# Kernel tuning notes

Measured on AMD Instinct MI355X. Metric: run time of the kernel, lower is better.

## Reference

```python
import jax, jax.numpy as jnp
import numpy as np

FEATURES = 1024
HEAD_DIM = 64
NUM_HEADS = 16
EPS = 1e-5


def setup_inputs() -> dict:
    key = jax.random.key(0)
    ks = jax.random.split(key, 6)
    x = jax.random.normal(ks[0], (2, 2048, FEATURES), dtype=jnp.float32)
    s_in = 1.0 / np.sqrt(FEATURES)
    s_hd = 1.0 / np.sqrt(NUM_HEADS * HEAD_DIM)
    return {
        "x": x,
        "gamma": jnp.ones((FEATURES,), jnp.float32),
        "beta": jnp.zeros((FEATURES,), jnp.float32),
        "Wq": jax.random.normal(ks[1], (FEATURES, NUM_HEADS * HEAD_DIM), jnp.float32) * s_in,
        "Wkv": jax.random.normal(ks[2], (FEATURES, 2 * HEAD_DIM), jnp.float32) * s_in,
        "Wo": jax.random.normal(ks[3], (NUM_HEADS * HEAD_DIM, FEATURES), jnp.float32) * s_hd,
        "bo": jax.random.normal(ks[4], (FEATURES,), jnp.float32) * s_hd,
    }


def reference(x, gamma, beta, Wq, Wkv, Wo, bo):
    # LayerNorm over last dim
    mu = jnp.mean(x, axis=-1, keepdims=True)
    var = jnp.mean(jnp.square(x - mu), axis=-1, keepdims=True)
    xn = (x - mu) * jax.lax.rsqrt(var + EPS) * gamma + beta

    b, t, _ = x.shape
    q = (xn @ Wq).reshape(b, t, NUM_HEADS, HEAD_DIM).transpose(0, 2, 1, 3)  # b h t d
    kv = xn @ Wkv  # b s 2d
    k, v = kv[..., :HEAD_DIM], kv[..., HEAD_DIM:]  # b s d (single shared head)

    scale = HEAD_DIM ** (-0.5)
    attn = jnp.einsum('bhtd,bsd->bhts', q, k) * scale
    attn = jax.nn.softmax(attn, axis=-1)
    out = jnp.einsum('bhts,bsd->bhtd', attn, v)
    out = out.transpose(0, 2, 1, 3).reshape(b, t, NUM_HEADS * HEAD_DIM)
    return out @ Wo + bo + x
```

## Files before the change

kernel.cpp:

```cpp
#include <hip/hip_runtime.h>

typedef __attribute__((ext_vector_type(8))) __bf16 bf16x8;
typedef __attribute__((ext_vector_type(4))) float floatx4;
typedef __attribute__((ext_vector_type(2))) unsigned int u32x2;
typedef unsigned short u16;
typedef unsigned int u32;

#define KSCALE 0.18033688011112042f

__device__ __forceinline__ u16 f2bf(float f) {
    union { float f; u32 u; } v; v.f = f;
    u32 r = v.u + 0x7fffu + ((v.u >> 16) & 1u);
    return (u16)(r >> 16);
}

__device__ __forceinline__ u32 pk2bf(float a, float b) {
    union { float f; u32 u; } x, y; x.f = a; y.f = b;
    return __builtin_amdgcn_perm(y.u + 0x8000u, x.u + 0x8000u, 0x07060302);
}

__device__ __forceinline__ void gl_lds16(const u16* g, u16* l) {
    __builtin_amdgcn_global_load_lds((const __attribute__((address_space(1))) void*)g,
                                     (__attribute__((address_space(3))) void*)l, 16, 0, 0);
}

__global__ __launch_bounds__(256) void transpose3(const float* __restrict__ Wq, const float* __restrict__ Wkv,
                                                  const float* __restrict__ Wo, u16* __restrict__ WqkvT,
                                                  u16* __restrict__ WoT) {
    const int z = blockIdx.z;
    const float* in = (z == 0) ? Wq : (z == 1 ? Wkv : Wo);
    u16* out = (z == 0) ? WqkvT : (z == 1 ? WqkvT + (size_t)1024 * 1024 : WoT);
    const int cols = (z == 1) ? 128 : 1024;
    const int tr = blockIdx.y * 64, tc = blockIdx.x * 64;
    if (tc >= cols) return;
    __shared__ float tile[64][68];
    const int t = threadIdx.x;
    for (int p = 0; p < 4; p++) {
        int ri = (t >> 4) + p * 16;
        int ci = (t & 15) * 4;
        float4 v = *(const float4*)&in[(size_t)(tr + ri) * cols + tc + ci];
        tile[ri][ci + 0] = v.x; tile[ri][ci + 1] = v.y;
        tile[ri][ci + 2] = v.z; tile[ri][ci + 3] = v.w;
    }
    __syncthreads();
    for (int p = 0; p < 4; p++) {
        int oc = (t >> 4) + p * 16;
        int ir = (t & 15) * 4;
        float s = (z == 1 && (tc + oc) < 64) ? KSCALE : 1.0f;
        ushort4 o;
        o.x = f2bf(tile[ir + 0][oc] * s);
        o.y = f2bf(tile[ir + 1][oc] * s);
        o.z = f2bf(tile[ir + 2][oc] * s);
        o.w = f2bf(tile[ir + 3][oc] * s);
        *(ushort4*)&out[(size_t)(tc + oc) * 1024 + tr + ir] = o;
    }
}

__global__ __launch_bounds__(256) void ln_kernel(const float* __restrict__ x, const float* __restrict__ gamma,
                                                 const float* __restrict__ beta, u16* __restrict__ xn) {
    const int row = blockIdx.x, t = threadIdx.x;
    const float* xr = x + (size_t)row * 1024;
    float4 v = *(const float4*)&xr[t * 4];
    float s = v.x + v.y + v.z + v.w;
    float s2 = v.x * v.x + v.y * v.y + v.z * v.z + v.w * v.w;
    for (int off = 1; off < 64; off <<= 1) {
        s += __shfl_xor(s, off, 64);
        s2 += __shfl_xor(s2, off, 64);
    }
    __shared__ float ps[4], ps2[4];
    int w = t >> 6, lane = t & 63;
    if (lane == 0) { ps[w] = s; ps2[w] = s2; }
    __syncthreads();
    float S = ps[0] + ps[1] + ps[2] + ps[3];
    float S2 = ps2[0] + ps2[1] + ps2[2] + ps2[3];
    float mu = S * (1.0f / 1024.0f);
    float var = S2 * (1.0f / 1024.0f) - mu * mu;
    float rstd = rsqrtf(var + 1e-5f);
    ushort4 o;
    o.x = f2bf((v.x - mu) * rstd * gamma[t * 4 + 0] + beta[t * 4 + 0]);
    o.y = f2bf((v.y - mu) * rstd * gamma[t * 4 + 1] + beta[t * 4 + 1]);
    o.z = f2bf((v.z - mu) * rstd * gamma[t * 4 + 2] + beta[t * 4 + 2]);
    o.w = f2bf((v.w - mu) * rstd * gamma[t * 4 + 3] + beta[t * 4 + 3]);
    *(ushort4*)&xn[(size_t)row * 1024 + t * 4] = o;
}

template <bool FINAL>
__global__ __launch_bounds__(256) void gemm_bt(const u16* __restrict__ A, const u16* __restrict__ BT,
                                               u16* __restrict__ Cb, float* __restrict__ Cf,
                                               const float* __restrict__ bias, const float* __restrict__ resid,
                                               int M, int N, int K) {
    __shared__ u16 as_[64 * 32];
    __shared__ u16 bs_[128 * 32];
    const int t = threadIdx.x;
    const int w = t >> 6, lane = t & 63, q = lane >> 4, c = lane & 15;
    const int tm = blockIdx.y * 64, tn = blockIdx.x * 128;
    const int wm = (w & 1) * 32, wn = (w >> 1) * 64;

    const int srow = lane >> 2, sch = lane & 3;
    const u16* ag = &A[(size_t)(tm + w * 16 + srow) * K + sch * 8];
    const u16* bg0 = &BT[(size_t)(tn + w * 32 + srow) * K + sch * 8];
    const u16* bg1 = &BT[(size_t)(tn + w * 32 + 16 + srow) * K + sch * 8];
    u16* al = &as_[(w * 16) * 32];
    u16* bl0 = &bs_[(w * 32) * 32];
    u16* bl1 = &bs_[(w * 32 + 16) * 32];

    floatx4 acc[2][4];
    for (int i = 0; i < 2; i++)
        for (int j = 0; j < 4; j++) acc[i][j] = (floatx4){0.f, 0.f, 0.f, 0.f};

    for (int k0 = 0; k0 < K; k0 += 32) {
        __syncthreads();
        gl_lds16(ag + k0, al);
        gl_lds16(bg0 + k0, bl0);
        gl_lds16(bg1 + k0, bl1);
        __syncthreads();
        bf16x8 af[2], bf[4];
#pragma unroll
        for (int i = 0; i < 2; i++) af[i] = *(const bf16x8*)&as_[(wm + i * 16 + c) * 32 + q * 8];
#pragma unroll
        for (int j = 0; j < 4; j++) bf[j] = *(const bf16x8*)&bs_[(wn + j * 16 + c) * 32 + q * 8];
#pragma unroll
        for (int i = 0; i < 2; i++)
#pragma unroll
            for (int j = 0; j < 4; j++)
                acc[i][j] = __builtin_amdgcn_mfma_f32_16x16x32_bf16(af[i], bf[j], acc[i][j], 0, 0, 0);
    }
#pragma unroll
    for (int i = 0; i < 2; i++)
#pragma unroll
        for (int j = 0; j < 4; j++)
#pragma unroll
            for (int r = 0; r < 4; r++) {
                int row = tm + wm + i * 16 + q * 4 + r;
                int col = tn + wn + j * 16 + c;
                if (FINAL)
                    Cf[(size_t)row * N + col] = acc[i][j][r] + bias[col] + resid[(size_t)row * N + col];
                else
                    Cb[(size_t)row * N + col] = f2bf(acc[i][j][r]);
            }
}

__global__ __launch_bounds__(256) void vt_prep(const u16* __restrict__ qkv, u16* __restrict__ vt) {
    __shared__ u16 tile[64][72];
    const int t = threadIdx.x;
    const int s0 = blockIdx.x * 64, b = blockIdx.y;
    for (int i = 0; i < 2; i++) {
        int ch = t + i * 256;
        int sl = ch >> 3, d0 = (ch & 7) * 8;
        *(uint4*)&tile[sl][d0] = *(const uint4*)&qkv[(size_t)(b * 2048 + s0 + sl) * 1152 + 1088 + d0];
    }
    __syncthreads();
    for (int i = 0; i < 2; i++) {
        int ch = t + i * 256;
        int d = ch >> 3, sl0 = (ch & 7) * 8;
        u16 tmp[8];
        for (int j = 0; j < 8; j++) tmp[j] = tile[sl0 + j][d];
        *(uint4*)&vt[((size_t)b * 64 + d) * 2048 + s0 + sl0] = *(uint4*)tmp;
    }
}

union Vf { bf16x8 v; u32 w[4]; };

__global__ __launch_bounds__(256, 2) void attn4(const u16* __restrict__ qkv, const u16* __restrict__ vt,
                                                u16* __restrict__ out) {
    __shared__ u16 ksm[2][64 * 64];
    __shared__ u16 vsm[2][64 * 64];
    const int t = threadIdx.x;
    const int w = t >> 6, lane = t & 63;
    const int q = lane >> 4, c = lane & 15;
    const int qt = blockIdx.x, hg = blockIdx.y, b = blockIdx.z;
    const int h = hg * 4 + w;
    const size_t qrow0 = (size_t)b * 2048 + qt * 32;
    const u16* kbase = qkv + (size_t)b * 2048 * 1152 + 1024;
    const u16* vbase = vt + (size_t)b * 64 * 2048;

    const int sr = w * 16 + (lane >> 3);
    const int sch = lane & 7;
    const int swz = (sch ^ (sr & 7)) * 8;
    const u16* kg0 = kbase + (size_t)sr * 1152 + swz;
    const u16* kg1 = kbase + (size_t)(sr + 8) * 1152 + swz;
    const u16* vg0 = vbase + (size_t)sr * 2048 + swz;
    const u16* vg1 = vbase + (size_t)(sr + 8) * 2048 + swz;
    u16* kl0[2] = {&ksm[0][(w * 16) * 64], &ksm[1][(w * 16) * 64]};
    u16* kl1[2] = {&ksm[0][(w * 16 + 8) * 64], &ksm[1][(w * 16 + 8) * 64]};
    u16* vl0[2] = {&vsm[0][(w * 16) * 64], &vsm[1][(w * 16) * 64]};
    u16* vl1[2] = {&vsm[0][(w * 16 + 8) * 64], &vsm[1][(w * 16 + 8) * 64]};

    bf16x8 qf[2][2];
#pragma unroll
    for (int mi = 0; mi < 2; mi++)
#pragma unroll
        for (int kk = 0; kk < 2; kk++)
            qf[mi][kk] = *(const bf16x8*)&qkv[(qrow0 + mi * 16 + c) * 1152 + h * 64 + kk * 32 + q * 8];

    floatx4 O[4][2], Lacc[2];
#pragma unroll
    for (int di = 0; di < 4; di++)
#pragma unroll
        for (int mi = 0; mi < 2; mi++) O[di][mi] = (floatx4){0.f, 0.f, 0.f, 0.f};
    Lacc[0] = (floatx4){0.f, 0.f, 0.f, 0.f};
    Lacc[1] = (floatx4){0.f, 0.f, 0.f, 0.f};
    Vf ones;
    ones.w[0] = ones.w[1] = ones.w[2] = ones.w[3] = 0x3F803F80u;

    gl_lds16(kg0, kl0[0]);
    gl_lds16(kg1, kl1[0]);
    gl_lds16(vg0, vl0[0]);
    gl_lds16(vg1, vl1[0]);
    __syncthreads();

    const int c7 = c & 7;
    for (int tt = 0; tt < 32; tt++) {
        const int cur = tt & 1, nxt = cur ^ 1;
        if (tt < 31) {
            const size_t ko = (size_t)(tt + 1) * 64 * 1152;
            const int vo = (tt + 1) * 64;
            gl_lds16(kg0 + ko, kl0[nxt]);
            gl_lds16(kg1 + ko, kl1[nxt]);
            gl_lds16(vg0 + vo, vl0[nxt]);
            gl_lds16(vg1 + vo, vl1[nxt]);
        }

        bf16x8 kf[4][2];
        Vf vf[4][2];
#pragma unroll
        for (int ni = 0; ni < 4; ni++)
#pragma unroll
            for (int kk = 0; kk < 2; kk++)
                kf[ni][kk] = *(const bf16x8*)&ksm[cur][(ni * 16 + c) * 64 + (((kk * 4 + q) ^ c7) * 8)];
#pragma unroll
        for (int di = 0; di < 4; di++)
#pragma unroll
            for (int kk = 0; kk < 2; kk++) {
                *(u32x2*)&vf[di][kk].w[0] =
                    *(const u32x2*)&vsm[cur][(di * 16 + c) * 64 + (((kk * 4 + (q >> 1)) ^ c7) * 8) + (q & 1) * 4];
                *(u32x2*)&vf[di][kk].w[2] =
                    *(const u32x2*)&vsm[cur][(di * 16 + c) * 64 + (((kk * 4 + 2 + (q >> 1)) ^ c7) * 8) + (q & 1) * 4];
            }

        floatx4 sacc[4][2];
#pragma unroll
        for (int ni = 0; ni < 4; ni++)
#pragma unroll
            for (int mi = 0; mi < 2; mi++) {
                floatx4 z = (floatx4){0.f, 0.f, 0.f, 0.f};
                z = __builtin_amdgcn_mfma_f32_16x16x32_bf16(kf[ni][0], qf[mi][0], z, 0, 0, 0);
                z = __builtin_amdgcn_mfma_f32_16x16x32_bf16(kf[ni][1], qf[mi][1], z, 0, 0, 0);
                sacc[ni][mi] = z;
            }

        u32 pk[4][2][2];
#pragma unroll
        for (int mi = 0; mi < 2; mi++)
#pragma unroll
            for (int ni = 0; ni < 4; ni++) {
                float p0 = exp2f(sacc[ni][mi][0]);
                float p1 = exp2f(sacc[ni][mi][1]);
                float p2 = exp2f(sacc[ni][mi][2]);
                float p3 = exp2f(sacc[ni][mi][3]);
                pk[ni][mi][0] = pk2bf(p0, p1);
                pk[ni][mi][1] = pk2bf(p2, p3);
            }

#pragma unroll
        for (int kk = 0; kk < 2; kk++) {
            Vf pf[2];
#pragma unroll
            for (int mi = 0; mi < 2; mi++) {
                pf[mi].w[0] = pk[2 * kk][mi][0];
                pf[mi].w[1] = pk[2 * kk][mi][1];
                pf[mi].w[2] = pk[2 * kk + 1][mi][0];
                pf[mi].w[3] = pk[2 * kk + 1][mi][1];
            }
#pragma unroll
            for (int di = 0; di < 4; di++)
#pragma unroll
                for (int mi = 0; mi < 2; mi++)
                    O[di][mi] = __builtin_amdgcn_mfma_f32_16x16x32_bf16(vf[di][kk].v, pf[mi].v, O[di][mi], 0, 0, 0);
#pragma unroll
            for (int mi = 0; mi < 2; mi++)
                Lacc[mi] = __builtin_amdgcn_mfma_f32_16x16x32_bf16(ones.v, pf[mi].v, Lacc[mi], 0, 0, 0);
        }

        __syncthreads();
    }

    float inv[2] = {1.0f / Lacc[0][0], 1.0f / Lacc[1][0]};
#pragma unroll
    for (int di = 0; di < 4; di++)
#pragma unroll
        for (int mi = 0; mi < 2; mi++) {
            ushort4 o;
            o.x = f2bf(O[di][mi][0] * inv[mi]);
            o.y = f2bf(O[di][mi][1] * inv[mi]);
            o.z = f2bf(O[di][mi][2] * inv[mi]);
            o.w = f2bf(O[di][mi][3] * inv[mi]);
            *(ushort4*)&out[(qrow0 + mi * 16 + c) * 1024 + h * 64 + di * 16 + q * 4] = o;
        }
}

extern "C" void kernel_launch(void* const* d_in, const int* in_sizes, int n_in,
                              void* d_out, int out_size, void* d_ws, size_t ws_size,
                              hipStream_t stream) {
    const float* x = (const float*)d_in[0];
    const float* gamma = (const float*)d_in[1];
    const float* beta = (const float*)d_in[2];
    const float* Wq = (const float*)d_in[3];
    const float* Wkv = (const float*)d_in[4];
    const float* Wo = (const float*)d_in[5];
    const float* bo = (const float*)d_in[6];
    float* out = (float*)d_out;

    u16* WqkvT = (u16*)d_ws;
    u16* WoT = WqkvT + (size_t)1152 * 1024;
    u16* xn = WoT + (size_t)1024 * 1024;
    u16* qkv = xn + (size_t)4096 * 1024;
    u16* attnO = xn;
    u16* Vt = WqkvT;

    transpose3<<<dim3(16, 16, 3), 256, 0, stream>>>(Wq, Wkv, Wo, WqkvT, WoT);
    ln_kernel<<<4096, 256, 0, stream>>>(x, gamma, beta, xn);
    gemm_bt<false><<<dim3(9, 64), 256, 0, stream>>>(xn, WqkvT, qkv, nullptr, nullptr, nullptr,
                                                    4096, 1152, 1024);
    vt_prep<<<dim3(32, 2), 256, 0, stream>>>(qkv, Vt);
    attn4<<<dim3(64, 4, 2), 256, 0, stream>>>(qkv, Vt, attnO);
    gemm_bt<true><<<dim3(8, 64), 256, 0, stream>>>(attnO, WoT, nullptr, out, bo, x,
                                                   4096, 1024, 1024);
}
```

Baseline: 199.2 us.

## Merge prep kernels, fuse V transpose into QKV GEMM, retile GEMM and attention

Combines the weight-transpose and LayerNorm kernels into one launch. The QKV GEMM epilogue now writes V directly into a permuted transposed layout, which removes the separate vt_prep kernel and its extra pass over V. The GEMM tile grows from 64x128 to 128x128 so each block does more MFMA work per B tile loaded. Attention moves to 512-thread blocks with 16 query rows per wave and a single 16-byte V fragment read, giving more waves per block and fewer LDS loads. The trade-offs are more accumulator registers in the GEMM and only half as many GEMM blocks.

```diff
diff --git a/kernel.cpp b/kernel.cpp
--- a/kernel.cpp
+++ b/kernel.cpp
@@ -2,7 +2,6 @@
 
 typedef __attribute__((ext_vector_type(8))) __bf16 bf16x8;
 typedef __attribute__((ext_vector_type(4))) float floatx4;
-typedef __attribute__((ext_vector_type(2))) unsigned int u32x2;
 typedef unsigned short u16;
 typedef unsigned int u32;
 
@@ -24,144 +23,138 @@
                                      (__attribute__((address_space(3))) void*)l, 16, 0, 0);
 }
 
-__global__ __launch_bounds__(256) void transpose3(const float* __restrict__ Wq, const float* __restrict__ Wkv,
-                                                  const float* __restrict__ Wo, u16* __restrict__ WqkvT,
-                                                  u16* __restrict__ WoT) {
-    const int z = blockIdx.z;
-    const float* in = (z == 0) ? Wq : (z == 1 ? Wkv : Wo);
-    u16* out = (z == 0) ? WqkvT : (z == 1 ? WqkvT + (size_t)1024 * 1024 : WoT);
-    const int cols = (z == 1) ? 128 : 1024;
-    const int tr = blockIdx.y * 64, tc = blockIdx.x * 64;
-    if (tc >= cols) return;
+__global__ __launch_bounds__(256) void prep(const float* __restrict__ Wq, const float* __restrict__ Wkv,
+                                            const float* __restrict__ Wo, const float* __restrict__ x,
+                                            const float* __restrict__ gamma, const float* __restrict__ beta,
+                                            u16* __restrict__ WqkvT, u16* __restrict__ WoT,
+                                            u16* __restrict__ xn) {
     __shared__ float tile[64][68];
+    __shared__ float ps[4], ps2[4];
+    const int bx = blockIdx.x;
     const int t = threadIdx.x;
-    for (int p = 0; p < 4; p++) {
-        int ri = (t >> 4) + p * 16;
-        int ci = (t & 15) * 4;
-        float4 v = *(const float4*)&in[(size_t)(tr + ri) * cols + tc + ci];
-        tile[ri][ci + 0] = v.x; tile[ri][ci + 1] = v.y;
-        tile[ri][ci + 2] = v.z; tile[ri][ci + 3] = v.w;
-    }
-    __syncthreads();
-    for (int p = 0; p < 4; p++) {
-        int oc = (t >> 4) + p * 16;
-        int ir = (t & 15) * 4;
-        float s = (z == 1 && (tc + oc) < 64) ? KSCALE : 1.0f;
+    if (bx < 768) {
+        const int z = bx >> 8, rem = bx & 255;
+        const int tr = (rem >> 4) * 64, tc = (rem & 15) * 64;
+        const float* in = (z == 0) ? Wq : (z == 1 ? Wkv : Wo);
+        u16* out = (z == 0) ? WqkvT : (z == 1 ? WqkvT + (size_t)1024 * 1024 : WoT);
+        const int cols = (z == 1) ? 128 : 1024;
+        if (tc >= cols) return;
+        for (int p = 0; p < 4; p++) {
+            int ri = (t >> 4) + p * 16;
+            int ci = (t & 15) * 4;
+            float4 v = *(const float4*)&in[(size_t)(tr + ri) * cols + tc + ci];
+            tile[ri][ci + 0] = v.x; tile[ri][ci + 1] = v.y;
+            tile[ri][ci + 2] = v.z; tile[ri][ci + 3] = v.w;
+        }
+        __syncthreads();
+        for (int p = 0; p < 4; p++) {
+            int oc = (t >> 4) + p * 16;
+            int ir = (t & 15) * 4;
+            float s = (z == 1 && (tc + oc) < 64) ? KSCALE : 1.0f;
+            ushort4 o;
+            o.x = f2bf(tile[ir + 0][oc] * s);
+            o.y = f2bf(tile[ir + 1][oc] * s);
+            o.z = f2bf(tile[ir + 2][oc] * s);
+            o.w = f2bf(tile[ir + 3][oc] * s);
+            *(ushort4*)&out[(size_t)(tc + oc) * 1024 + tr + ir] = o;
+        }
+    } else {
+        const int row = bx - 768;
+        const float* xr = x + (size_t)row * 1024;
+        float4 v = *(const float4*)&xr[t * 4];
+        float s = v.x + v.y + v.z + v.w;
+        float s2 = v.x * v.x + v.y * v.y + v.z * v.z + v.w * v.w;
+        for (int off = 1; off < 64; off <<= 1) {
+            s += __shfl_xor(s, off, 64);
+            s2 += __shfl_xor(s2, off, 64);
+        }
+        int w = t >> 6, lane = t & 63;
+        if (lane == 0) { ps[w] = s; ps2[w] = s2; }
+        __syncthreads();
+        float S = ps[0] + ps[1] + ps[2] + ps[3];
+        float S2 = ps2[0] + ps2[1] + ps2[2] + ps2[3];
+        float mu = S * (1.0f / 1024.0f);
+        float var = S2 * (1.0f / 1024.0f) - mu * mu;
+        float rstd = rsqrtf(var + 1e-5f);
         ushort4 o;
-        o.x = f2bf(tile[ir + 0][oc] * s);
-        o.y = f2bf(tile[ir + 1][oc] * s);
-        o.z = f2bf(tile[ir + 2][oc] * s);
-        o.w = f2bf(tile[ir + 3][oc] * s);
-        *(ushort4*)&out[(size_t)(tc + oc) * 1024 + tr + ir] = o;
-    }
-}
-
-__global__ __launch_bounds__(256) void ln_kernel(const float* __restrict__ x, const float* __restrict__ gamma,
-                                                 const float* __restrict__ beta, u16* __restrict__ xn) {
-    const int row = blockIdx.x, t = threadIdx.x;
-    const float* xr = x + (size_t)row * 1024;
-    float4 v = *(const float4*)&xr[t * 4];
-    float s = v.x + v.y + v.z + v.w;
-    float s2 = v.x * v.x + v.y * v.y + v.z * v.z + v.w * v.w;
-    for (int off = 1; off < 64; off <<= 1) {
-        s += __shfl_xor(s, off, 64);
-        s2 += __shfl_xor(s2, off, 64);
-    }
-    __shared__ float ps[4], ps2[4];
-    int w = t >> 6, lane = t & 63;
-    if (lane == 0) { ps[w] = s; ps2[w] = s2; }
-    __syncthreads();
-    float S = ps[0] + ps[1] + ps[2] + ps[3];
-    float S2 = ps2[0] + ps2[1] + ps2[2] + ps2[3];
-    float mu = S * (1.0f / 1024.0f);
-    float var = S2 * (1.0f / 1024.0f) - mu * mu;
-    float rstd = rsqrtf(var + 1e-5f);
-    ushort4 o;
-    o.x = f2bf((v.x - mu) * rstd * gamma[t * 4 + 0] + beta[t * 4 + 0]);
-    o.y = f2bf((v.y - mu) * rstd * gamma[t * 4 + 1] + beta[t * 4 + 1]);
-    o.z = f2bf((v.z - mu) * rstd * gamma[t * 4 + 2] + beta[t * 4 + 2]);
-    o.w = f2bf((v.w - mu) * rstd * gamma[t * 4 + 3] + beta[t * 4 + 3]);
-    *(ushort4*)&xn[(size_t)row * 1024 + t * 4] = o;
+        o.x = f2bf((v.x - mu) * rstd * gamma[t * 4 + 0] + beta[t * 4 + 0]);
+        o.y = f2bf((v.y - mu) * rstd * gamma[t * 4 + 1] + beta[t * 4 + 1]);
+        o.z = f2bf((v.z - mu) * rstd * gamma[t * 4 + 2] + beta[t * 4 + 2]);
+        o.w = f2bf((v.w - mu) * rstd * gamma[t * 4 + 3] + beta[t * 4 + 3]);
+        *(ushort4*)&xn[(size_t)row * 1024 + t * 4] = o;
+    }
 }
 
 template <bool FINAL>
 __global__ __launch_bounds__(256) void gemm_bt(const u16* __restrict__ A, const u16* __restrict__ BT,
                                                u16* __restrict__ Cb, float* __restrict__ Cf,
                                                const float* __restrict__ bias, const float* __restrict__ resid,
-                                               int M, int N, int K) {
-    __shared__ u16 as_[64 * 32];
+                                               u16* __restrict__ vt2, int M, int N, int K) {
+    __shared__ u16 as_[128 * 32];
     __shared__ u16 bs_[128 * 32];
     const int t = threadIdx.x;
     const int w = t >> 6, lane = t & 63, q = lane >> 4, c = lane & 15;
-    const int tm = blockIdx.y * 64, tn = blockIdx.x * 128;
-    const int wm = (w & 1) * 32, wn = (w >> 1) * 64;
-
-    const int srow = lane >> 2, sch = lane & 3;
-    const u16* ag = &A[(size_t)(tm + w * 16 + srow) * K + sch * 8];
-    const u16* bg0 = &BT[(size_t)(tn + w * 32 + srow) * K + sch * 8];
-    const u16* bg1 = &BT[(size_t)(tn + w * 32 + 16 + srow) * K + sch * 8];
-    u16* al = &as_[(w * 16) * 32];
-    u16* bl0 = &bs_[(w * 32) * 32];
-    u16* bl1 = &bs_[(w * 32 + 16) * 32];
-
-    floatx4 acc[2][4];
-    for (int i = 0; i < 2; i++)
+    const int tm = blockIdx.y * 128, tn = blockIdx.x * 128;
+    const int wm = (w & 1) * 64, wn = (w >> 1) * 64;
+
+    const int srow = lane >> 2, sch = (lane & 3) * 8;
+    const u16* ag0 = A + (size_t)(tm + w * 16 + srow) * K + sch;
+    const u16* ag1 = ag0 + (size_t)64 * K;
+    const u16* bg0 = BT + (size_t)(tn + w * 16 + srow) * K + sch;
+    const u16* bg1 = bg0 + (size_t)64 * K;
+    u16* al0 = as_ + (w * 16) * 32;
+    u16* al1 = as_ + (64 + w * 16) * 32;
+    u16* bl0 = bs_ + (w * 16) * 32;
+    u16* bl1 = bs_ + (64 + w * 16) * 32;
+
+    floatx4 acc[4][4];
+    for (int i = 0; i < 4; i++)
         for (int j = 0; j < 4; j++) acc[i][j] = (floatx4){0.f, 0.f, 0.f, 0.f};
 
     for (int k0 = 0; k0 < K; k0 += 32) {
         __syncthreads();
-        gl_lds16(ag + k0, al);
+        gl_lds16(ag0 + k0, al0);
+        gl_lds16(ag1 + k0, al1);
         gl_lds16(bg0 + k0, bl0);
         gl_lds16(bg1 + k0, bl1);
         __syncthreads();
-        bf16x8 af[2], bf[4];
-#pragma unroll
-        for (int i = 0; i < 2; i++) af[i] = *(const bf16x8*)&as_[(wm + i * 16 + c) * 32 + q * 8];
+        bf16x8 af[4], bf[4];
+#pragma unroll
+        for (int i = 0; i < 4; i++) af[i] = *(const bf16x8*)&as_[(wm + i * 16 + c) * 32 + q * 8];
 #pragma unroll
         for (int j = 0; j < 4; j++) bf[j] = *(const bf16x8*)&bs_[(wn + j * 16 + c) * 32 + q * 8];
 #pragma unroll
-        for (int i = 0; i < 2; i++)
+        for (int i = 0; i < 4; i++)
 #pragma unroll
             for (int j = 0; j < 4; j++)
                 acc[i][j] = __builtin_amdgcn_mfma_f32_16x16x32_bf16(af[i], bf[j], acc[i][j], 0, 0, 0);
     }
 #pragma unroll
-    for (int i = 0; i < 2; i++)
+    for (int i = 0; i < 4; i++)
 #pragma unroll
         for (int j = 0; j < 4; j++)
 #pragma unroll
             for (int r = 0; r < 4; r++) {
                 int row = tm + wm + i * 16 + q * 4 + r;
                 int col = tn + wn + j * 16 + c;
-                if (FINAL)
-                    Cf[(size_t)row * N + col] = acc[i][j][r] + bias[col] + resid[(size_t)row * N + col];
-                else
-                    Cb[(size_t)row * N + col] = f2bf(acc[i][j][r]);
+                float v = acc[i][j][r];
+                if (FINAL) {
+                    Cf[(size_t)row * N + col] = v + bias[col] + resid[(size_t)row * N + col];
+                } else if (col < 1088) {
+                    Cb[(size_t)row * N + col] = f2bf(v);
+                } else {
+                    int d = col - 1088;
+                    int bb = row >> 11, sl = row & 2047;
+                    int Bk = sl >> 5, u = sl & 31;
+                    int up = ((u >> 2) & 3) * 8 + ((u >> 4) << 2) + (u & 3);
+                    vt2[((size_t)(bb * 64 + d)) * 2048 + Bk * 32 + up] = f2bf(v);
+                }
             }
 }
 
-__global__ __launch_bounds__(256) void vt_prep(const u16* __restrict__ qkv, u16* __restrict__ vt) {
-    __shared__ u16 tile[64][72];
-    const int t = threadIdx.x;
-    const int s0 = blockIdx.x * 64, b = blockIdx.y;
-    for (int i = 0; i < 2; i++) {
-        int ch = t + i * 256;
-        int sl = ch >> 3, d0 = (ch & 7) * 8;
-        *(uint4*)&tile[sl][d0] = *(const uint4*)&qkv[(size_t)(b * 2048 + s0 + sl) * 1152 + 1088 + d0];
-    }
-    __syncthreads();
-    for (int i = 0; i < 2; i++) {
-        int ch = t + i * 256;
-        int d = ch >> 3, sl0 = (ch & 7) * 8;
-        u16 tmp[8];
-        for (int j = 0; j < 8; j++) tmp[j] = tile[sl0 + j][d];
-        *(uint4*)&vt[((size_t)b * 64 + d) * 2048 + s0 + sl0] = *(uint4*)tmp;
-    }
-}
-
 union Vf { bf16x8 v; u32 w[4]; };
 
-__global__ __launch_bounds__(256, 2) void attn4(const u16* __restrict__ qkv, const u16* __restrict__ vt,
+__global__ __launch_bounds__(512, 4) void attn5(const u16* __restrict__ qkv, const u16* __restrict__ vt2,
                                                 u16* __restrict__ out) {
     __shared__ u16 ksm[2][64 * 64];
     __shared__ u16 vsm[2][64 * 64];
@@ -169,56 +162,41 @@
     const int w = t >> 6, lane = t & 63;
     const int q = lane >> 4, c = lane & 15;
     const int qt = blockIdx.x, hg = blockIdx.y, b = blockIdx.z;
-    const int h = hg * 4 + w;
-    const size_t qrow0 = (size_t)b * 2048 + qt * 32;
+    const int h = hg * 8 + w;
+    const size_t qrow0 = (size_t)b * 2048 + qt * 16;
     const u16* kbase = qkv + (size_t)b * 2048 * 1152 + 1024;
-    const u16* vbase = vt + (size_t)b * 64 * 2048;
-
-    const int sr = w * 16 + (lane >> 3);
+    const u16* vbase = vt2 + (size_t)b * 64 * 2048;
+
+    const int srow = w * 8 + (lane >> 3);
     const int sch = lane & 7;
-    const int swz = (sch ^ (sr & 7)) * 8;
-    const u16* kg0 = kbase + (size_t)sr * 1152 + swz;
-    const u16* kg1 = kbase + (size_t)(sr + 8) * 1152 + swz;
-    const u16* vg0 = vbase + (size_t)sr * 2048 + swz;
-    const u16* vg1 = vbase + (size_t)(sr + 8) * 2048 + swz;
-    u16* kl0[2] = {&ksm[0][(w * 16) * 64], &ksm[1][(w * 16) * 64]};
-    u16* kl1[2] = {&ksm[0][(w * 16 + 8) * 64], &ksm[1][(w * 16 + 8) * 64]};
-    u16* vl0[2] = {&vsm[0][(w * 16) * 64], &vsm[1][(w * 16) * 64]};
-    u16* vl1[2] = {&vsm[0][(w * 16 + 8) * 64], &vsm[1][(w * 16 + 8) * 64]};
-
-    bf16x8 qf[2][2];
-#pragma unroll
-    for (int mi = 0; mi < 2; mi++)
-#pragma unroll
-        for (int kk = 0; kk < 2; kk++)
-            qf[mi][kk] = *(const bf16x8*)&qkv[(qrow0 + mi * 16 + c) * 1152 + h * 64 + kk * 32 + q * 8];
-
-    floatx4 O[4][2], Lacc[2];
-#pragma unroll
-    for (int di = 0; di < 4; di++)
-#pragma unroll
-        for (int mi = 0; mi < 2; mi++) O[di][mi] = (floatx4){0.f, 0.f, 0.f, 0.f};
-    Lacc[0] = (floatx4){0.f, 0.f, 0.f, 0.f};
-    Lacc[1] = (floatx4){0.f, 0.f, 0.f, 0.f};
+    const int swz = (sch ^ (srow & 7)) * 8;
+    const u16* kg = kbase + (size_t)srow * 1152 + swz;
+    const u16* vg = vbase + (size_t)srow * 2048 + swz;
+    u16* kl[2] = {&ksm[0][(w * 8) * 64], &ksm[1][(w * 8) * 64]};
+    u16* vl[2] = {&vsm[0][(w * 8) * 64], &vsm[1][(w * 8) * 64]};
+
+    bf16x8 qf[2];
+#pragma unroll
+    for (int kk = 0; kk < 2; kk++)
+        qf[kk] = *(const bf16x8*)&qkv[(qrow0 + c) * 1152 + h * 64 + kk * 32 + q * 8];
+
+    floatx4 O[4], Lacc;
+#pragma unroll
+    for (int di = 0; di < 4; di++) O[di] = (floatx4){0.f, 0.f, 0.f, 0.f};
+    Lacc = (floatx4){0.f, 0.f, 0.f, 0.f};
     Vf ones;
     ones.w[0] = ones.w[1] = ones.w[2] = ones.w[3] = 0x3F803F80u;
 
-    gl_lds16(kg0, kl0[0]);
-    gl_lds16(kg1, kl1[0]);
-    gl_lds16(vg0, vl0[0]);
-    gl_lds16(vg1, vl1[0]);
+    gl_lds16(kg, kl[0]);
+    gl_lds16(vg, vl[0]);
     __syncthreads();
 
     const int c7 = c & 7;
     for (int tt = 0; tt < 32; tt++) {
         const int cur = tt & 1, nxt = cur ^ 1;
         if (tt < 31) {
-            const size_t ko = (size_t)(tt + 1) * 64 * 1152;
-            const int vo = (tt + 1) * 64;
-            gl_lds16(kg0 + ko, kl0[nxt]);
-            gl_lds16(kg1 + ko, kl1[nxt]);
-            gl_lds16(vg0 + vo, vl0[nxt]);
-            gl_lds16(vg1 + vo, vl1[nxt]);
+            gl_lds16(kg + (size_t)(tt + 1) * 64 * 1152, kl[nxt]);
+            gl_lds16(vg + (tt + 1) * 64, vl[nxt]);
         }
 
         bf16x8 kf[4][2];
@@ -231,72 +209,55 @@
 #pragma unroll
         for (int di = 0; di < 4; di++)
 #pragma unroll
-            for (int kk = 0; kk < 2; kk++) {
-                *(u32x2*)&vf[di][kk].w[0] =
-                    *(const u32x2*)&vsm[cur][(di * 16 + c) * 64 + (((kk * 4 + (q >> 1)) ^ c7) * 8) + (q & 1) * 4];
-                *(u32x2*)&vf[di][kk].w[2] =
-                    *(const u32x2*)&vsm[cur][(di * 16 + c) * 64 + (((kk * 4 + 2 + (q >> 1)) ^ c7) * 8) + (q & 1) * 4];
-            }
-
-        floatx4 sacc[4][2];
-#pragma unroll
-        for (int ni = 0; ni < 4; ni++)
-#pragma unroll
-            for (int mi = 0; mi < 2; mi++) {
-                floatx4 z = (floatx4){0.f, 0.f, 0.f, 0.f};
-                z = __builtin_amdgcn_mfma_f32_16x16x32_bf16(kf[ni][0], qf[mi][0], z, 0, 0, 0);
-                z = __builtin_amdgcn_mfma_f32_16x16x32_bf16(kf[ni][1], qf[mi][1], z, 0, 0, 0);
-                sacc[ni][mi] = z;
-            }
-
-        u32 pk[4][2][2];
-#pragma unroll
-        for (int mi = 0; mi < 2; mi++)
-#pragma unroll
-            for (int ni = 0; ni < 4; ni++) {
-                float p0 = exp2f(sacc[ni][mi][0]);
-                float p1 = exp2f(sacc[ni][mi][1]);
-                float p2 = exp2f(sacc[ni][mi][2]);
-                float p3 = exp2f(sacc[ni][mi][3]);
-                pk[ni][mi][0] = pk2bf(p0, p1);
-                pk[ni][mi][1] = pk2bf(p2, p3);
-            }
+            for (int kk = 0; kk < 2; kk++)
+                vf[di][kk].v = *(const bf16x8*)&vsm[cur][(di * 16 + c) * 64 + (((kk * 4 + q) ^ c7) * 8)];
+
+        floatx4 sacc[4];
+#pragma unroll
+        for (int ni = 0; ni < 4; ni++) {
+            floatx4 z = (floatx4){0.f, 0.f, 0.f, 0.f};
+            z = __builtin_amdgcn_mfma_f32_16x16x32_bf16(kf[ni][0], qf[0], z, 0, 0, 0);
+            z = __builtin_amdgcn_mfma_f32_16x16x32_bf16(kf[ni][1], qf[1], z, 0, 0, 0);
+            sacc[ni] = z;
+        }
+
+        u32 pk[4][2];
+#pragma unroll
+        for (int ni = 0; ni < 4; ni++) {
+            float p0 = exp2f(sacc[ni][0]);
+            float p1 = exp2f(sacc[ni][1]);
+            float p2 = exp2f(sacc[ni][2]);
+            float p3 = exp2f(sacc[ni][3]);
+            pk[ni][0] = pk2bf(p0, p1);
+            pk[ni][1] = pk2bf(p2, p3);
+        }
 
 #pragma unroll
         for (int kk = 0; kk < 2; kk++) {
-            Vf pf[2];
-#pragma unroll
-            for (int mi = 0; mi < 2; mi++) {
-                pf[mi].w[0] = pk[2 * kk][mi][0];
-                pf[mi].w[1] = pk[2 * kk][mi][1];
-                pf[mi].w[2] = pk[2 * kk + 1][mi][0];
-                pf[mi].w[3] = pk[2 * kk + 1][mi][1];
-            }
+            Vf pf;
+            pf.w[0] = pk[2 * kk][0];
+            pf.w[1] = pk[2 * kk][1];
+            pf.w[2] = pk[2 * kk + 1][0];
+            pf.w[3] = pk[2 * kk + 1][1];
 #pragma unroll
             for (int di = 0; di < 4; di++)
-#pragma unroll
-                for (int mi = 0; mi < 2; mi++)
-                    O[di][mi] = __builtin_amdgcn_mfma_f32_16x16x32_bf16(vf[di][kk].v, pf[mi].v, O[di][mi], 0, 0, 0);
-#pragma unroll
-            for (int mi = 0; mi < 2; mi++)
-                Lacc[mi] = __builtin_amdgcn_mfma_f32_16x16x32_bf16(ones.v, pf[mi].v, Lacc[mi], 0, 0, 0);
-        }
-
-        __syncthreads();
-    }
-
-    float inv[2] = {1.0f / Lacc[0][0], 1.0f / Lacc[1][0]};
-#pragma unroll
-    for (int di = 0; di < 4; di++)
-#pragma unroll
-        for (int mi = 0; mi < 2; mi++) {
-            ushort4 o;
-            o.x = f2bf(O[di][mi][0] * inv[mi]);
-            o.y = f2bf(O[di][mi][1] * inv[mi]);
-            o.z = f2bf(O[di][mi][2] * inv[mi]);
-            o.w = f2bf(O[di][mi][3] * inv[mi]);
-            *(ushort4*)&out[(qrow0 + mi * 16 + c) * 1024 + h * 64 + di * 16 + q * 4] = o;
-        }
+                O[di] = __builtin_amdgcn_mfma_f32_16x16x32_bf16(vf[di][kk].v, pf.v, O[di], 0, 0, 0);
+            Lacc = __builtin_amdgcn_mfma_f32_16x16x32_bf16(ones.v, pf.v, Lacc, 0, 0, 0);
+        }
+
+        __syncthreads();
+    }
+
+    float inv = 1.0f / Lacc[0];
+#pragma unroll
+    for (int di = 0; di < 4; di++) {
+        ushort4 o;
+        o.x = f2bf(O[di][0] * inv);
+        o.y = f2bf(O[di][1] * inv);
+        o.z = f2bf(O[di][2] * inv);
+        o.w = f2bf(O[di][3] * inv);
+        *(ushort4*)&out[(qrow0 + c) * 1024 + h * 64 + di * 16 + q * 4] = o;
+    }
 }
 
 extern "C" void kernel_launch(void* const* d_in, const int* in_sizes, int n_in,
@@ -315,15 +276,13 @@
     u16* WoT = WqkvT + (size_t)1152 * 1024;
     u16* xn = WoT + (size_t)1024 * 1024;
     u16* qkv = xn + (size_t)4096 * 1024;
+    u16* vt2 = qkv + (size_t)4096 * 1152;
     u16* attnO = xn;
-    u16* Vt = WqkvT;
-
-    transpose3<<<dim3(16, 16, 3), 256, 0, stream>>>(Wq, Wkv, Wo, WqkvT, WoT);
-    ln_kernel<<<4096, 256, 0, stream>>>(x, gamma, beta, xn);
-    gemm_bt<false><<<dim3(9, 64), 256, 0, stream>>>(xn, WqkvT, qkv, nullptr, nullptr, nullptr,
+
+    prep<<<4864, 256, 0, stream>>>(Wq, Wkv, Wo, x, gamma, beta, WqkvT, WoT, xn);
+    gemm_bt<false><<<dim3(9, 32), 256, 0, stream>>>(xn, WqkvT, qkv, nullptr, nullptr, nullptr, vt2,
                                                     4096, 1152, 1024);
-    vt_prep<<<dim3(32, 2), 256, 0, stream>>>(qkv, Vt);
-    attn4<<<dim3(64, 4, 2), 256, 0, stream>>>(qkv, Vt, attnO);
-    gemm_bt<true><<<dim3(8, 64), 256, 0, stream>>>(attnO, WoT, nullptr, out, bo, x,
+    attn5<<<dim3(128, 2, 2), 512, 0, stream>>>(qkv, vt2, attnO);
+    gemm_bt<true><<<dim3(8, 32), 256, 0, stream>>>(attnO, WoT, nullptr, out, bo, x, nullptr,
                                                    4096, 1024, 1024);
 }
```

After: 199.9 us. No clear change (+0.4%).

## Fuse prep kernels, widen GEMM K-tile with swizzle, emit permuted V^T from QKV GEMM

Applied to the files above, without the earlier changes.

Merges the weight transpose and LayerNorm into one prep launch. The GEMM now loads 64-wide K tiles with an XOR-swizzled LDS layout, halving barrier count per K. The QKV GEMM epilogue writes V directly in a transposed, permuted layout, so the separate vt_prep kernel goes away and attention can read V fragments with single 16-byte LDS loads. This cuts launches and a pass over V. In exchange it adds scattered 2-byte stores in the V epilogue and doubles LDS per GEMM block, which may lower occupancy.

```diff
diff --git a/kernel.cpp b/kernel.cpp
--- a/kernel.cpp
+++ b/kernel.cpp
@@ -2,7 +2,6 @@
 
 typedef __attribute__((ext_vector_type(8))) __bf16 bf16x8;
 typedef __attribute__((ext_vector_type(4))) float floatx4;
-typedef __attribute__((ext_vector_type(2))) unsigned int u32x2;
 typedef unsigned short u16;
 typedef unsigned int u32;
 
@@ -24,106 +23,130 @@
                                      (__attribute__((address_space(3))) void*)l, 16, 0, 0);
 }
 
-__global__ __launch_bounds__(256) void transpose3(const float* __restrict__ Wq, const float* __restrict__ Wkv,
-                                                  const float* __restrict__ Wo, u16* __restrict__ WqkvT,
-                                                  u16* __restrict__ WoT) {
-    const int z = blockIdx.z;
-    const float* in = (z == 0) ? Wq : (z == 1 ? Wkv : Wo);
-    u16* out = (z == 0) ? WqkvT : (z == 1 ? WqkvT + (size_t)1024 * 1024 : WoT);
-    const int cols = (z == 1) ? 128 : 1024;
-    const int tr = blockIdx.y * 64, tc = blockIdx.x * 64;
-    if (tc >= cols) return;
+__global__ __launch_bounds__(256) void prep(const float* __restrict__ Wq, const float* __restrict__ Wkv,
+                                            const float* __restrict__ Wo, const float* __restrict__ x,
+                                            const float* __restrict__ gamma, const float* __restrict__ beta,
+                                            u16* __restrict__ WqkvT, u16* __restrict__ WoT,
+                                            u16* __restrict__ xn) {
     __shared__ float tile[64][68];
+    __shared__ float ps[4], ps2[4];
+    const int bx = blockIdx.x;
     const int t = threadIdx.x;
-    for (int p = 0; p < 4; p++) {
-        int ri = (t >> 4) + p * 16;
-        int ci = (t & 15) * 4;
-        float4 v = *(const float4*)&in[(size_t)(tr + ri) * cols + tc + ci];
-        tile[ri][ci + 0] = v.x; tile[ri][ci + 1] = v.y;
-        tile[ri][ci + 2] = v.z; tile[ri][ci + 3] = v.w;
+    if (bx < 768) {
+        const int z = bx >> 8, rem = bx & 255;
+        const int tr = (rem >> 4) * 64, tc = (rem & 15) * 64;
+        const float* in = (z == 0) ? Wq : (z == 1 ? Wkv : Wo);
+        u16* out = (z == 0) ? WqkvT : (z == 1 ? WqkvT + (size_t)1024 * 1024 : WoT);
+        const int cols = (z == 1) ? 128 : 1024;
+        if (tc >= cols) return;
+        for (int p = 0; p < 4; p++) {
+            int ri = (t >> 4) + p * 16;
+            int ci = (t & 15) * 4;
+            float4 v = *(const float4*)&in[(size_t)(tr + ri) * cols + tc + ci];
+            tile[ri][ci + 0] = v.x; tile[ri][ci + 1] = v.y;
+            tile[ri][ci + 2] = v.z; tile[ri][ci + 3] = v.w;
+        }
+        __syncthreads();
+        for (int p = 0; p < 4; p++) {
+            int oc = (t >> 4) + p * 16;
+            int ir = (t & 15) * 4;
+            float s = (z == 1 && (tc + oc) < 64) ? KSCALE : 1.0f;
+            ushort4 o;
+            o.x = f2bf(tile[ir + 0][oc] * s);
+            o.y = f2bf(tile[ir + 1][oc] * s);
+            o.z = f2bf(tile[ir + 2][oc] * s);
+            o.w = f2bf(tile[ir + 3][oc] * s);
+            *(ushort4*)&out[(size_t)(tc + oc) * 1024 + tr + ir] = o;
+        }
+    } else {
+        const int row = bx - 768;
+        const float* xr = x + (size_t)row * 1024;
+        float4 v = *(const float4*)&xr[t * 4];
+        float s = v.x + v.y + v.z + v.w;
+        float s2 = v.x * v.x + v.y * v.y + v.z * v.z + v.w * v.w;
+        for (int off = 1; off < 64; off <<= 1) {
+            s += __shfl_xor(s, off, 64);
+            s2 += __shfl_xor(s2, off, 64);
+        }
+        int w = t >> 6, lane = t & 63;
+        if (lane == 0) { ps[w] = s; ps2[w] = s2; }
+        __syncthreads();
+        float S = ps[0] + ps[1] + ps[2] + ps[3];
+        float S2 = ps2[0] + ps2[1] + ps2[2] + ps2[3];
+        float mu = S * (1.0f / 1024.0f);
+        float var = S2 * (1.0f / 1024.0f) - mu * mu;
+        float rstd = rsqrtf(var + 1e-5f);
+        ushort4 o;
+        o.x = f2bf((v.x - mu) * rstd * gamma[t * 4 + 0] + beta[t * 4 + 0]);
+        o.y = f2bf((v.y - mu) * rstd * gamma[t * 4 + 1] + beta[t * 4 + 1]);
+        o.z = f2bf((v.z - mu) * rstd * gamma[t * 4 + 2] + beta[t * 4 + 2]);
+        o.w = f2bf((v.w - mu) * rstd * gamma[t * 4 + 3] + beta[t * 4 + 3]);
+        *(ushort4*)&xn[(size_t)row * 1024 + t * 4] = o;
     }
-    __syncthreads();
-    for (int p = 0; p < 4; p++) {
-        int oc = (t >> 4) + p * 16;
-        int ir = (t & 15) * 4;
-        float s = (z == 1 && (tc + oc) < 64) ? KSCALE : 1.0f;
-        ushort4 o;
-        o.x = f2bf(tile[ir + 0][oc] * s);
-        o.y = f2bf(tile[ir + 1][oc] * s);
-        o.z = f2bf(tile[ir + 2][oc] * s);
-        o.w = f2bf(tile[ir + 3][oc] * s);
-        *(ushort4*)&out[(size_t)(tc + oc) * 1024 + tr + ir] = o;
-    }
-}
-
-__global__ __launch_bounds__(256) void ln_kernel(const float* __restrict__ x, const float* __restrict__ gamma,
-                                                 const float* __restrict__ beta, u16* __restrict__ xn) {
-    const int row = blockIdx.x, t = threadIdx.x;
-    const float* xr = x + (size_t)row * 1024;
-    float4 v = *(const float4*)&xr[t * 4];
-    float s = v.x + v.y + v.z + v.w;
-    float s2 = v.x * v.x + v.y * v.y + v.z * v.z + v.w * v.w;
-    for (int off = 1; off < 64; off <<= 1) {
-        s += __shfl_xor(s, off, 64);
-        s2 += __shfl_xor(s2, off, 64);
-    }
-    __shared__ float ps[4], ps2[4];
-    int w = t >> 6, lane = t & 63;
-    if (lane == 0) { ps[w] = s; ps2[w] = s2; }
-    __syncthreads();
-    float S = ps[0] + ps[1] + ps[2] + ps[3];
-    float S2 = ps2[0] + ps2[1] + ps2[2] + ps2[3];
-    float mu = S * (1.0f / 1024.0f);
-    float var = S2 * (1.0f / 1024.0f) - mu * mu;
-    float rstd = rsqrtf(var + 1e-5f);
-    ushort4 o;
-    o.x = f2bf((v.x - mu) * rstd * gamma[t * 4 + 0] + beta[t * 4 + 0]);
-    o.y = f2bf((v.y - mu) * rstd * gamma[t * 4 + 1] + beta[t * 4 + 1]);
-    o.z = f2bf((v.z - mu) * rstd * gamma[t * 4 + 2] + beta[t * 4 + 2]);
-    o.w = f2bf((v.w - mu) * rstd * gamma[t * 4 + 3] + beta[t * 4 + 3]);
-    *(ushort4*)&xn[(size_t)row * 1024 + t * 4] = o;
 }
 
 template <bool FINAL>
 __global__ __launch_bounds__(256) void gemm_bt(const u16* __restrict__ A, const u16* __restrict__ BT,
                                                u16* __restrict__ Cb, float* __restrict__ Cf,
                                                const float* __restrict__ bias, const float* __restrict__ resid,
-                                               int M, int N, int K) {
-    __shared__ u16 as_[64 * 32];
-    __shared__ u16 bs_[128 * 32];
+                                               u16* __restrict__ vt2, int M, int N, int K) {
+    __shared__ u16 as_[64 * 64];
+    __shared__ u16 bs_[128 * 64];
     const int t = threadIdx.x;
     const int w = t >> 6, lane = t & 63, q = lane >> 4, c = lane & 15;
     const int tm = blockIdx.y * 64, tn = blockIdx.x * 128;
     const int wm = (w & 1) * 32, wn = (w >> 1) * 64;
 
-    const int srow = lane >> 2, sch = lane & 3;
-    const u16* ag = &A[(size_t)(tm + w * 16 + srow) * K + sch * 8];
-    const u16* bg0 = &BT[(size_t)(tn + w * 32 + srow) * K + sch * 8];
-    const u16* bg1 = &BT[(size_t)(tn + w * 32 + 16 + srow) * K + sch * 8];
-    u16* al = &as_[(w * 16) * 32];
-    u16* bl0 = &bs_[(w * 32) * 32];
-    u16* bl1 = &bs_[(w * 32 + 16) * 32];
+    const int l3 = lane >> 3, sch = lane & 7;
+    const int arow = w * 16 + l3;
+    const int aswz = (sch ^ (arow & 7)) * 8;
+    const int brow = w * 32 + l3;
+    const int bswz = (sch ^ (brow & 7)) * 8;
+    const u16* ag0 = A + (size_t)(tm + arow) * K + aswz;
+    const u16* ag1 = ag0 + (size_t)8 * K;
+    const u16* bg0 = BT + (size_t)(tn + brow) * K + bswz;
+    const u16* bg1 = bg0 + (size_t)8 * K;
+    const u16* bg2 = bg0 + (size_t)16 * K;
+    const u16* bg3 = bg0 + (size_t)24 * K;
+    u16* al0 = as_ + (w * 16) * 64;
+    u16* al1 = as_ + (w * 16 + 8) * 64;
+    u16* bl0 = bs_ + (w * 32) * 64;
+    u16* bl1 = bs_ + (w * 32 + 8) * 64;
+    u16* bl2 = bs_ + (w * 32 + 16) * 64;
+    u16* bl3 = bs_ + (w * 32 + 24) * 64;
 
     floatx4 acc[2][4];
     for (int i = 0; i < 2; i++)
         for (int j = 0; j < 4; j++) acc[i][j] = (floatx4){0.f, 0.f, 0.f, 0.f};
 
-    for (int k0 = 0; k0 < K; k0 += 32) {
-        __syncthreads();
-        gl_lds16(ag + k0, al);
+    const int c7 = c & 7;
+    for (int k0 = 0; k0 < K; k0 += 64) {
+        __syncthreads();
+        gl_lds16(ag0 + k0, al0);
+        gl_lds16(ag1 + k0, al1);
         gl_lds16(bg0 + k0, bl0);
         gl_lds16(bg1 + k0, bl1);
-        __syncthreads();
-        bf16x8 af[2], bf[4];
-#pragma unroll
-        for (int i = 0; i < 2; i++) af[i] = *(const bf16x8*)&as_[(wm + i * 16 + c) * 32 + q * 8];
-#pragma unroll
-        for (int j = 0; j < 4; j++) bf[j] = *(const bf16x8*)&bs_[(wn + j * 16 + c) * 32 + q * 8];
+        gl_lds16(bg2 + k0, bl2);
+        gl_lds16(bg3 + k0, bl3);
+        __syncthreads();
+        bf16x8 af[2][2], bf[4][2];
 #pragma unroll
         for (int i = 0; i < 2; i++)
 #pragma unroll
-            for (int j = 0; j < 4; j++)
-                acc[i][j] = __builtin_amdgcn_mfma_f32_16x16x32_bf16(af[i], bf[j], acc[i][j], 0, 0, 0);
+            for (int kk = 0; kk < 2; kk++)
+                af[i][kk] = *(const bf16x8*)&as_[(wm + i * 16 + c) * 64 + (((kk * 4 + q) ^ c7) * 8)];
+#pragma unroll
+        for (int j = 0; j < 4; j++)
+#pragma unroll
+            for (int kk = 0; kk < 2; kk++)
+                bf[j][kk] = *(const bf16x8*)&bs_[(wn + j * 16 + c) * 64 + (((kk * 4 + q) ^ c7) * 8)];
+#pragma unroll
+        for (int kk = 0; kk < 2; kk++)
+#pragma unroll
+            for (int i = 0; i < 2; i++)
+#pragma unroll
+                for (int j = 0; j < 4; j++)
+                    acc[i][j] = __builtin_amdgcn_mfma_f32_16x16x32_bf16(af[i][kk], bf[j][kk], acc[i][j], 0, 0, 0);
     }
 #pragma unroll
     for (int i = 0; i < 2; i++)
@@ -133,35 +156,24 @@
             for (int r = 0; r < 4; r++) {
                 int row = tm + wm + i * 16 + q * 4 + r;
                 int col = tn + wn + j * 16 + c;
-                if (FINAL)
-                    Cf[(size_t)row * N + col] = acc[i][j][r] + bias[col] + resid[(size_t)row * N + col];
-                else
-                    Cb[(size_t)row * N + col] = f2bf(acc[i][j][r]);
+                float v = acc[i][j][r];
+                if (FINAL) {
+                    Cf[(size_t)row * N + col] = v + bias[col] + resid[(size_t)row * N + col];
+                } else if (col < 1088) {
+                    Cb[(size_t)row * N + col] = f2bf(v);
+                } else {
+                    int d = col - 1088;
+                    int bb = row >> 11, sl = row & 2047;
+                    int Bk = sl >> 5, u = sl & 31;
+                    int up = ((u >> 2) & 3) * 8 + ((u >> 4) << 2) + (u & 3);
+                    vt2[((size_t)(bb * 64 + d)) * 2048 + Bk * 32 + up] = f2bf(v);
+                }
             }
 }
 
-__global__ __launch_bounds__(256) void vt_prep(const u16* __restrict__ qkv, u16* __restrict__ vt) {
-    __shared__ u16 tile[64][72];
-    const int t = threadIdx.x;
-    const int s0 = blockIdx.x * 64, b = blockIdx.y;
-    for (int i = 0; i < 2; i++) {
-        int ch = t + i * 256;
-        int sl = ch >> 3, d0 = (ch & 7) * 8;
-        *(uint4*)&tile[sl][d0] = *(const uint4*)&qkv[(size_t)(b * 2048 + s0 + sl) * 1152 + 1088 + d0];
-    }
-    __syncthreads();
-    for (int i = 0; i < 2; i++) {
-        int ch = t + i * 256;
-        int d = ch >> 3, sl0 = (ch & 7) * 8;
-        u16 tmp[8];
-        for (int j = 0; j < 8; j++) tmp[j] = tile[sl0 + j][d];
-        *(uint4*)&vt[((size_t)b * 64 + d) * 2048 + s0 + sl0] = *(uint4*)tmp;
-    }
-}
-
 union Vf { bf16x8 v; u32 w[4]; };
 
-__global__ __launch_bounds__(256, 2) void attn4(const u16* __restrict__ qkv, const u16* __restrict__ vt,
+__global__ __launch_bounds__(256, 2) void attn7(const u16* __restrict__ qkv, const u16* __restrict__ vt2,
                                                 u16* __restrict__ out) {
     __shared__ u16 ksm[2][64 * 64];
     __shared__ u16 vsm[2][64 * 64];
@@ -172,15 +184,15 @@
     const int h = hg * 4 + w;
     const size_t qrow0 = (size_t)b * 2048 + qt * 32;
     const u16* kbase = qkv + (size_t)b * 2048 * 1152 + 1024;
-    const u16* vbase = vt + (size_t)b * 64 * 2048;
-
-    const int sr = w * 16 + (lane >> 3);
-    const int sch = lane & 7;
-    const int swz = (sch ^ (sr & 7)) * 8;
-    const u16* kg0 = kbase + (size_t)sr * 1152 + swz;
-    const u16* kg1 = kbase + (size_t)(sr + 8) * 1152 + swz;
-    const u16* vg0 = vbase + (size_t)sr * 2048 + swz;
-    const u16* vg1 = vbase + (size_t)(sr + 8) * 2048 + swz;
+    const u16* vbase = vt2 + (size_t)b * 64 * 2048;
+
+    const int l3 = lane >> 3, sch = lane & 7;
+    const int srow = w * 16 + l3;
+    const int swz = (sch ^ (srow & 7)) * 8;
+    const u16* kg0 = kbase + (size_t)srow * 1152 + swz;
+    const u16* kg1 = kg0 + (size_t)8 * 1152;
+    const u16* vg0 = vbase + (size_t)srow * 2048 + swz;
+    const u16* vg1 = vg0 + (size_t)8 * 2048;
     u16* kl0[2] = {&ksm[0][(w * 16) * 64], &ksm[1][(w * 16) * 64]};
     u16* kl1[2] = {&ksm[0][(w * 16 + 8) * 64], &ksm[1][(w * 16 + 8) * 64]};
     u16* vl0[2] = {&vsm[0][(w * 16) * 64], &vsm[1][(w * 16) * 64]};
@@ -231,12 +243,8 @@
 #pragma unroll
         for (int di = 0; di < 4; di++)
 #pragma unroll
-            for (int kk = 0; kk < 2; kk++) {
-                *(u32x2*)&vf[di][kk].w[0] =
-                    *(const u32x2*)&vsm[cur][(di * 16 + c) * 64 + (((kk * 4 + (q >> 1)) ^ c7) * 8) + (q & 1) * 4];
-                *(u32x2*)&vf[di][kk].w[2] =
-                    *(const u32x2*)&vsm[cur][(di * 16 + c) * 64 + (((kk * 4 + 2 + (q >> 1)) ^ c7) * 8) + (q & 1) * 4];
-            }
+            for (int kk = 0; kk < 2; kk++)
+                vf[di][kk].v = *(const bf16x8*)&vsm[cur][(di * 16 + c) * 64 + (((kk * 4 + q) ^ c7) * 8)];
 
         floatx4 sacc[4][2];
 #pragma unroll
@@ -315,15 +323,13 @@
     u16* WoT = WqkvT + (size_t)1152 * 1024;
     u16* xn = WoT + (size_t)1024 * 1024;
     u16* qkv = xn + (size_t)4096 * 1024;
+    u16* vt2 = qkv + (size_t)4096 * 1152;
     u16* attnO = xn;
-    u16* Vt = WqkvT;
-
-    transpose3<<<dim3(16, 16, 3), 256, 0, stream>>>(Wq, Wkv, Wo, WqkvT, WoT);
-    ln_kernel<<<4096, 256, 0, stream>>>(x, gamma, beta, xn);
-    gemm_bt<false><<<dim3(9, 64), 256, 0, stream>>>(xn, WqkvT, qkv, nullptr, nullptr, nullptr,
+
+    prep<<<4864, 256, 0, stream>>>(Wq, Wkv, Wo, x, gamma, beta, WqkvT, WoT, xn);
+    gemm_bt<false><<<dim3(9, 64), 256, 0, stream>>>(xn, WqkvT, qkv, nullptr, nullptr, nullptr, vt2,
                                                     4096, 1152, 1024);
-    vt_prep<<<dim3(32, 2), 256, 0, stream>>>(qkv, Vt);
-    attn4<<<dim3(64, 4, 2), 256, 0, stream>>>(qkv, Vt, attnO);
-    gemm_bt<true><<<dim3(8, 64), 256, 0, stream>>>(attnO, WoT, nullptr, out, bo, x,
+    attn7<<<dim3(64, 4, 2), 256, 0, stream>>>(qkv, vt2, attnO);
+    gemm_bt<true><<<dim3(8, 64), 256, 0, stream>>>(attnO, WoT, nullptr, out, bo, x, nullptr,
                                                    4096, 1024, 1024);
 }
```

New measurement: 182.5 us. 1.09x faster.
